# Kernel tuning notes

Measured on AMD Instinct MI355X. Metric: run time of the kernel, lower is better.

## Reference

```python
import jax, jax.numpy as jnp
import numpy as np

LEAKY_SLOPE = 0.2
LN_EPS = 1e-5


def _leaky_relu(x):
    return jnp.where(x >= 0, x, LEAKY_SLOPE * x)


def _layer_norm(x, gamma, beta):
    mean = jnp.mean(x, axis=-1, keepdims=True)
    var = jnp.var(x, axis=-1, keepdims=True)
    return (x - mean) * jax.lax.rsqrt(var + LN_EPS) * gamma + beta


def setup_inputs() -> dict:
    key = jax.random.key(0)
    ks = jax.random.split(key, 8)
    n_nodes, n_edges = 50000, 640000
    cin, cout = 128, 128
    x = jax.random.normal(ks[0], (n_nodes, cin), dtype=jnp.float32)
    edge_index = jax.random.randint(ks[1], (2, n_edges), 0, n_nodes, dtype=jnp.int64)
    # Linear weights stored torch-style [out, in]; init ~ U(-1/sqrt(fan_in), 1/sqrt(fan_in))
    def lin(k, fan_out, fan_in):
        b = 1.0 / np.sqrt(fan_in)
        return jax.random.uniform(k, (fan_out, fan_in), jnp.float32, -b, b)
    W1 = lin(ks[2], cout, 2 * cin)
    b1 = jax.random.uniform(ks[3], (cout,), jnp.float32, -1/np.sqrt(2*cin), 1/np.sqrt(2*cin))
    W2 = lin(ks[4], cout, cout)
    b2 = jax.random.uniform(ks[5], (cout,), jnp.float32, -1/np.sqrt(cout), 1/np.sqrt(cout))
    W3 = lin(ks[6], cout, cout)  # bias=False
    gamma = jnp.ones((cout,), jnp.float32)
    beta = jnp.zeros((cout,), jnp.float32)
    return {"x": x, "edge_index": edge_index, "W1": W1, "b1": b1,
            "W2": W2, "b2": b2, "W3": W3, "gamma": gamma, "beta": beta}


def reference(x, edge_index, W1, b1, W2, b2, W3, gamma, beta):
    src, dest = edge_index[0], edge_index[1]
    message = jnp.concatenate((x[dest], x[src]), axis=-1)  # [E, 2*cin]
    h = _leaky_relu(message @ W1.T + b1)
    h = _leaky_relu(h @ W2.T + b2)
    h = h @ W3.T
    return _layer_norm(h, gamma, beta)
```

## Files before the change

kernel.cpp:

```cpp
#include <hip/hip_runtime.h>

typedef unsigned short u16;
typedef unsigned int u32;
typedef __attribute__((ext_vector_type(8))) short bf16x8;
typedef __attribute__((ext_vector_type(4))) float f32x4;
typedef __attribute__((ext_vector_type(4))) u32 u32x4;

union U8 { u32 w[4]; u32x4 u4; bf16x8 v; };

#define LEAKY 0.2f
#define LN_EPS 1e-5f

__device__ __forceinline__ u16 f2bf(float f) {
  union { float f; u32 u; } a; a.f = f;
  return (u16)((a.u + 0x7fffu + ((a.u >> 16) & 1u)) >> 16);
}
__device__ __forceinline__ u32 pk2(float lo, float hi) {
  return (u32)f2bf(lo) | ((u32)f2bf(hi) << 16);
}
__device__ __forceinline__ u32x4 pack8(const f32x4& a, const f32x4& b) {
  u32x4 r;
  r[0] = pk2(a[0], a[1]); r[1] = pk2(a[2], a[3]);
  r[2] = pk2(b[0], b[1]); r[3] = pk2(b[2], b[3]);
  return r;
}

__global__ void build_wfrag(const float* __restrict__ W1,
                            const float* __restrict__ W2,
                            const float* __restrict__ W3,
                            u16* __restrict__ wout) {
  int id = blockIdx.x * 256 + threadIdx.x;
  int f = id >> 9, l = (id >> 3) & 63, i = id & 7;
  int p = l & 15, q = l >> 4, j = i & 3, h = i >> 2;
  const float* W; int c, K;
  if (f < 64)      { W = W1; c = f >> 3;        K = 256; }
  else if (f < 96) { W = W2; c = (f - 64) >> 3; K = 128; }
  else             { W = W3; c = (f - 96) >> 3; K = 128; }
  int n = f & 7;
  wout[id] = f2bf(W[(16 * n + p) * K + 32 * c + 4 * q + j + 16 * h]);
}

template <int FBASE>
__device__ __forceinline__ void gemm16(const u16* __restrict__ wlds, int lane,
                                       const U8* mf, f32x4* acc) {
  #pragma unroll
  for (int c = 0; c < 4; ++c) {
    #pragma unroll
    for (int n = 0; n < 8; ++n) {
      U8 wf;
      wf.v = *(const bf16x8*)(wlds + ((FBASE + c * 8 + n) << 9) + (lane << 3));
      acc[n] = __builtin_amdgcn_mfma_f32_16x16x32_bf16(wf.v, mf[c].v, acc[n], 0, 0, 0);
    }
  }
}

__device__ __forceinline__ void leaky_pack(f32x4* acc, U8* hf) {
  #pragma unroll
  for (int n = 0; n < 8; ++n) {
    #pragma unroll
    for (int j = 0; j < 4; ++j) {
      float v = acc[n][j];
      acc[n][j] = fmaxf(v, LEAKY * v);
    }
  }
  #pragma unroll
  for (int c = 0; c < 4; ++c) hf[c].u4 = pack8(acc[2 * c], acc[2 * c + 1]);
}

__device__ __forceinline__ u32 addleaky(u32 ua, u32 ub) {
  float alo = __uint_as_float(ua << 16);
  float ahi = __uint_as_float(ua & 0xFFFF0000u);
  float blo = __uint_as_float(ub << 16);
  float bhi = __uint_as_float(ub & 0xFFFF0000u);
  float lo = alo + blo, hi = ahi + bhi;
  lo = fmaxf(lo, LEAKY * lo);
  hi = fmaxf(hi, LEAKY * hi);
  return pk2(lo, hi);
}

__device__ __forceinline__ void ln_store(const f32x4* acc, const f32x4* gmf,
                                         const f32x4* btf, int q,
                                         float* __restrict__ orow) {
  float s = 0.f, ss = 0.f;
  #pragma unroll
  for (int n = 0; n < 8; ++n) {
    #pragma unroll
    for (int j = 0; j < 4; ++j) { float v = acc[n][j]; s += v; ss += v * v; }
  }
  s += __shfl_xor(s, 16, 64);  ss += __shfl_xor(ss, 16, 64);
  s += __shfl_xor(s, 32, 64);  ss += __shfl_xor(ss, 32, 64);
  float mean = s * (1.f / 128.f);
  float var  = fmaxf(ss * (1.f / 128.f) - mean * mean, 0.f);
  float inv  = rsqrtf(var + LN_EPS);
  #pragma unroll
  for (int n = 0; n < 8; ++n) {
    f32x4 gm = gmf[4 * n + q], bt = btf[4 * n + q];
    #pragma unroll
    for (int j = 0; j < 4; ++j)
      orow[16 * n + j] = (acc[n][j] - mean) * inv * gm[j] + bt[j];
  }
}

__global__ __launch_bounds__(512, 2) void node_pre(
    const float* __restrict__ x, const float* __restrict__ b1,
    const u16* __restrict__ wbf, u16* __restrict__ y, int NN) {
  __shared__ __align__(16) u16 wlds[32768];
  __shared__ __align__(16) float b1l[128];
  const int tid = threadIdx.x;
  {
    const uint4* s = (const uint4*)wbf;
    uint4* d = (uint4*)wlds;
    #pragma unroll
    for (int i = 0; i < 8; ++i) d[tid + i * 512] = s[tid + i * 512];
  }
  if (tid < 128) b1l[tid] = b1[tid];
  __syncthreads();

  const int lane = tid & 63, p = lane & 15, q = lane >> 4;
  const int wid = (blockIdx.x << 3) | (tid >> 6);
  const f32x4* b1f = (const f32x4*)b1l;
  const int NT = (NN + 15) >> 4;

  for (int t = wid; t < NT; t += 2048) {
    const int r = t * 16 + p;
    const int cr = r < NN ? r : NN - 1;
    U8 mf[4];
    #pragma unroll
    for (int c = 0; c < 4; ++c) {
      float4 a0 = *(const float4*)(x + (long)cr * 128 + 32 * c + 4 * q);
      float4 a1 = *(const float4*)(x + (long)cr * 128 + 32 * c + 4 * q + 16);
      mf[c].w[0] = pk2(a0.x, a0.y); mf[c].w[1] = pk2(a0.z, a0.w);
      mf[c].w[2] = pk2(a1.x, a1.y); mf[c].w[3] = pk2(a1.z, a1.w);
    }
    f32x4 ya[8], yb[8];
    #pragma unroll
    for (int n = 0; n < 8; ++n) {
      ya[n] = (f32x4)(0.f);
      yb[n] = b1f[4 * n + q];
    }
    gemm16<0>(wlds, lane, mf, ya);
    gemm16<32>(wlds, lane, mf, yb);
    #pragma unroll
    for (int c = 0; c < 4; ++c) {
      *(u32x4*)(y + (long)r * 256 + c * 32 + q * 8)       = pack8(ya[2*c], ya[2*c+1]);
      *(u32x4*)(y + (long)r * 256 + 128 + c * 32 + q * 8) = pack8(yb[2*c], yb[2*c+1]);
    }
  }
}

__global__ __launch_bounds__(512, 2) void edge_mlp_fac(
    const int* __restrict__ ei, const float* __restrict__ b2,
    const float* __restrict__ gamma, const float* __restrict__ beta,
    const u16* __restrict__ wbf, const u16* __restrict__ y,
    float* __restrict__ out, int E) {
  __shared__ __align__(16) u16 wlds[32768];
  __shared__ __align__(16) float parl[384];
  const int tid = threadIdx.x;
  {
    const uint4* s = (const uint4*)wbf;
    uint4* d = (uint4*)wlds;
    #pragma unroll
    for (int i = 0; i < 8; ++i) d[tid + i * 512] = s[tid + i * 512];
  }
  if (tid < 384) {
    int prm = tid >> 7, idx = tid & 127;
    const float* src = (prm == 0) ? b2 : (prm == 1) ? gamma : beta;
    parl[tid] = src[idx];
  }
  __syncthreads();

  const int lane = tid & 63, p = lane & 15, q = lane >> 4;
  const f32x4* pf = (const f32x4*)parl;
  const long ebase = (long)blockIdx.x * 512 + (tid >> 6) * 64;

  int nd[4], ns[4];
  #pragma unroll
  for (int i = 0; i < 4; ++i) {
    nd[i] = ei[E + ebase + i * 16 + p];
    ns[i] = ei[ebase + i * 16 + p];
  }

#define LOADY(A, B, node_d, node_s)                                   \
  { const u16* yd_ = y + (long)(node_d) * 256;                        \
    const u16* ys_ = y + (long)(node_s) * 256 + 128;                  \
    _Pragma("unroll")                                                 \
    for (int c = 0; c < 4; ++c) {                                     \
      A[c] = *(const u32x4*)(yd_ + c * 32 + q * 8);                   \
      B[c] = *(const u32x4*)(ys_ + c * 32 + q * 8);                   \
    } }

  auto compute_store = [&](const u32x4* ya, const u32x4* yb, int i) {
    U8 hf[4];
    #pragma unroll
    for (int c = 0; c < 4; ++c) {
      #pragma unroll
      for (int w2 = 0; w2 < 4; ++w2) hf[c].w[w2] = addleaky(ya[c][w2], yb[c][w2]);
    }
    f32x4 acc[8];
    #pragma unroll
    for (int n = 0; n < 8; ++n) acc[n] = pf[4 * n + q];
    gemm16<0>(wlds, lane, hf, acc);
    leaky_pack(acc, hf);
    #pragma unroll
    for (int n = 0; n < 8; ++n) acc[n] = (f32x4)(0.f);
    gemm16<32>(wlds, lane, hf, acc);
    ln_store(acc, pf + 32, pf + 64, q,
             out + (ebase + i * 16 + p) * 128 + 4 * q);
  };

  u32x4 a0[4], b0[4], a1[4], b1[4];
  LOADY(a0, b0, nd[0], ns[0]);
  LOADY(a1, b1, nd[1], ns[1]);
  compute_store(a0, b0, 0);
  LOADY(a0, b0, nd[2], ns[2]);
  compute_store(a1, b1, 1);
  LOADY(a1, b1, nd[3], ns[3]);
  compute_store(a0, b0, 2);
  compute_store(a1, b1, 3);
#undef LOADY
}

__global__ __launch_bounds__(512, 2) void edge_mlp_mono(
    const float* __restrict__ x, const int* __restrict__ ei,
    const float* __restrict__ b1, const float* __restrict__ b2,
    const float* __restrict__ gamma, const float* __restrict__ beta,
    const u16* __restrict__ wbf, float* __restrict__ out, int E) {
  __shared__ __align__(16) u16 wlds[65536];
  __shared__ __align__(16) float parl[512];
  const int tid = threadIdx.x;
  {
    const uint4* s = (const uint4*)wbf;
    uint4* d = (uint4*)wlds;
    #pragma unroll
    for (int i = 0; i < 16; ++i) d[tid + i * 512] = s[tid + i * 512];
  }
  if (tid < 512) {
    int prm = tid >> 7, idx = tid & 127;
    const float* src = (prm == 0) ? b1 : (prm == 1) ? b2 : (prm == 2) ? gamma : beta;
    parl[tid] = src[idx];
  }
  __syncthreads();

  const int lane = tid & 63, p = lane & 15, q = lane >> 4;
  const int wid = (blockIdx.x << 3) | (tid >> 6);
  const f32x4* pf = (const f32x4*)parl;
  const int NT = (E + 15) >> 4;

  for (int t = wid; t < NT; t += 2048) {
    const int e0 = t * 16;
    const int e = (e0 + p < E) ? e0 + p : E - 1;
    const int nd = ei[E + e], ns = ei[e];
    U8 mf[4];
    f32x4 acc[8];
    #pragma unroll
    for (int n = 0; n < 8; ++n) acc[n] = pf[4 * n + q];
    #pragma unroll
    for (int c = 0; c < 4; ++c) {
      float4 a0 = *(const float4*)(x + (long)nd * 128 + 32 * c + 4 * q);
      float4 a1 = *(const float4*)(x + (long)nd * 128 + 32 * c + 4 * q + 16);
      mf[c].w[0] = pk2(a0.x, a0.y); mf[c].w[1] = pk2(a0.z, a0.w);
      mf[c].w[2] = pk2(a1.x, a1.y); mf[c].w[3] = pk2(a1.z, a1.w);
    }
    gemm16<0>(wlds, lane, mf, acc);
    #pragma unroll
    for (int c = 0; c < 4; ++c) {
      float4 a0 = *(const float4*)(x + (long)ns * 128 + 32 * c + 4 * q);
      float4 a1 = *(const float4*)(x + (long)ns * 128 + 32 * c + 4 * q + 16);
      mf[c].w[0] = pk2(a0.x, a0.y); mf[c].w[1] = pk2(a0.z, a0.w);
      mf[c].w[2] = pk2(a1.x, a1.y); mf[c].w[3] = pk2(a1.z, a1.w);
    }
    gemm16<32>(wlds, lane, mf, acc);
    U8 hf[4];
    leaky_pack(acc, hf);
    #pragma unroll
    for (int n = 0; n < 8; ++n) acc[n] = pf[32 + 4 * n + q];
    gemm16<64>(wlds, lane, hf, acc);
    leaky_pack(acc, hf);
    #pragma unroll
    for (int n = 0; n < 8; ++n) acc[n] = (f32x4)(0.f);
    gemm16<96>(wlds, lane, hf, acc);
    if (e0 + p < E)
      ln_store(acc, pf + 64, pf + 96, q, out + (long)(e0 + p) * 128 + 4 * q);
  }
}

extern "C" void kernel_launch(void* const* d_in, const int* in_sizes, int n_in,
                              void* d_out, int out_size, void* d_ws, size_t ws_size,
                              hipStream_t stream) {
  const float* x     = (const float*)d_in[0];
  const int*   ei    = (const int*)d_in[1];
  const float* W1    = (const float*)d_in[2];
  const float* b1    = (const float*)d_in[3];
  const float* W2    = (const float*)d_in[4];
  const float* b2    = (const float*)d_in[5];
  const float* W3    = (const float*)d_in[6];
  const float* gamma = (const float*)d_in[7];
  const float* beta  = (const float*)d_in[8];
  const int E  = in_sizes[1] / 2;
  const int NN = in_sizes[0] / 128;

  const size_t npad    = ((size_t)(NN + 31) / 32) * 32;
  const size_t Y_BYTES = npad * 512;
  const size_t NEED    = Y_BYTES + 131072;

  if (ws_size >= NEED && (E % 512) == 0) {
    u16* y   = (u16*)d_ws;
    u16* wbf = (u16*)((char*)d_ws + Y_BYTES);
    build_wfrag<<<256, 256, 0, stream>>>(W1, W2, W3, wbf);
    node_pre<<<256, 512, 0, stream>>>(x, b1, wbf, y, NN);
    edge_mlp_fac<<<E / 512, 512, 0, stream>>>(ei, b2, gamma, beta, wbf + 32768,
                                              y, (float*)d_out, E);
  } else {
    u16* wbf = (u16*)d_ws;
    build_wfrag<<<256, 256, 0, stream>>>(W1, W2, W3, wbf);
    edge_mlp_mono<<<256, 512, 0, stream>>>(x, ei, b1, b2, gamma, beta, wbf,
                                           (float*)d_out, E);
  }
}
```

Measured before the change: 188.1 us.

## Process 1024 edges per block and issue first gathers before weight LDS load

Each block of edge_mlp_fac now handles 1024 edges instead of 512, with each wave processing eight 16-edge tiles in a double-buffered pipeline. Edge index loads are streamed just ahead of use rather than all preloaded. The first two gathers of node features are issued before the weight and parameter copy into LDS and the barrier, so gather latency overlaps the prologue. This halves the number of blocks and so the per-block cost of loading 64KB of weights into LDS. It also means fewer blocks for load balancing and requires E divisible by 1024; otherwise the slower fallback runs.

```diff
diff --git a/kernel.cpp b/kernel.cpp
--- a/kernel.cpp
+++ b/kernel.cpp
@@ -156,29 +156,9 @@
   __shared__ __align__(16) u16 wlds[32768];
   __shared__ __align__(16) float parl[384];
   const int tid = threadIdx.x;
-  {
-    const uint4* s = (const uint4*)wbf;
-    uint4* d = (uint4*)wlds;
-    #pragma unroll
-    for (int i = 0; i < 8; ++i) d[tid + i * 512] = s[tid + i * 512];
-  }
-  if (tid < 384) {
-    int prm = tid >> 7, idx = tid & 127;
-    const float* src = (prm == 0) ? b2 : (prm == 1) ? gamma : beta;
-    parl[tid] = src[idx];
-  }
-  __syncthreads();
-
   const int lane = tid & 63, p = lane & 15, q = lane >> 4;
   const f32x4* pf = (const f32x4*)parl;
-  const long ebase = (long)blockIdx.x * 512 + (tid >> 6) * 64;
-
-  int nd[4], ns[4];
-  #pragma unroll
-  for (int i = 0; i < 4; ++i) {
-    nd[i] = ei[E + ebase + i * 16 + p];
-    ns[i] = ei[ebase + i * 16 + p];
-  }
+  const long ebase = (long)blockIdx.x * 1024 + (tid >> 6) * 128;
 
 #define LOADY(A, B, node_d, node_s)                                   \
   { const u16* yd_ = y + (long)(node_d) * 256;                        \
@@ -189,6 +169,27 @@
       B[c] = *(const u32x4*)(ys_ + c * 32 + q * 8);                   \
     } }
 
+  int ndA = ei[E + ebase + p],      nsA = ei[ebase + p];
+  int ndB = ei[E + ebase + 16 + p], nsB = ei[ebase + 16 + p];
+  u32x4 a0[4], b0[4], a1[4], b1[4];
+  LOADY(a0, b0, ndA, nsA);
+  LOADY(a1, b1, ndB, nsB);
+  ndA = ei[E + ebase + 32 + p]; nsA = ei[ebase + 32 + p];
+  ndB = ei[E + ebase + 48 + p]; nsB = ei[ebase + 48 + p];
+
+  {
+    const uint4* s = (const uint4*)wbf;
+    uint4* d = (uint4*)wlds;
+    #pragma unroll
+    for (int i = 0; i < 8; ++i) d[tid + i * 512] = s[tid + i * 512];
+  }
+  if (tid < 384) {
+    int prm = tid >> 7, idx = tid & 127;
+    const float* src = (prm == 0) ? b2 : (prm == 1) ? gamma : beta;
+    parl[tid] = src[idx];
+  }
+  __syncthreads();
+
   auto compute_store = [&](const u32x4* ya, const u32x4* yb, int i) {
     U8 hf[4];
     #pragma unroll
@@ -208,15 +209,24 @@
              out + (ebase + i * 16 + p) * 128 + 4 * q);
   };
 
-  u32x4 a0[4], b0[4], a1[4], b1[4];
-  LOADY(a0, b0, nd[0], ns[0]);
-  LOADY(a1, b1, nd[1], ns[1]);
   compute_store(a0, b0, 0);
-  LOADY(a0, b0, nd[2], ns[2]);
+  LOADY(a0, b0, ndA, nsA);
+  ndA = ei[E + ebase + 64 + p]; nsA = ei[ebase + 64 + p];
   compute_store(a1, b1, 1);
-  LOADY(a1, b1, nd[3], ns[3]);
+  LOADY(a1, b1, ndB, nsB);
+  ndB = ei[E + ebase + 80 + p]; nsB = ei[ebase + 80 + p];
   compute_store(a0, b0, 2);
+  LOADY(a0, b0, ndA, nsA);
+  ndA = ei[E + ebase + 96 + p]; nsA = ei[ebase + 96 + p];
   compute_store(a1, b1, 3);
+  LOADY(a1, b1, ndB, nsB);
+  ndB = ei[E + ebase + 112 + p]; nsB = ei[ebase + 112 + p];
+  compute_store(a0, b0, 4);
+  LOADY(a0, b0, ndA, nsA);
+  compute_store(a1, b1, 5);
+  LOADY(a1, b1, ndB, nsB);
+  compute_store(a0, b0, 6);
+  compute_store(a1, b1, 7);
 #undef LOADY
 }
 
@@ -303,13 +313,13 @@
   const size_t Y_BYTES = npad * 512;
   const size_t NEED    = Y_BYTES + 131072;
 
-  if (ws_size >= NEED && (E % 512) == 0) {
+  if (ws_size >= NEED && (E % 1024) == 0) {
     u16* y   = (u16*)d_ws;
     u16* wbf = (u16*)((char*)d_ws + Y_BYTES);
     build_wfrag<<<256, 256, 0, stream>>>(W1, W2, W3, wbf);
     node_pre<<<256, 512, 0, stream>>>(x, b1, wbf, y, NN);
-    edge_mlp_fac<<<E / 512, 512, 0, stream>>>(ei, b2, gamma, beta, wbf + 32768,
-                                              y, (float*)d_out, E);
+    edge_mlp_fac<<<E / 1024, 512, 0, stream>>>(ei, b2, gamma, beta,
+                                               wbf + 32768, y, (float*)d_out, E);
   } else {
     u16* wbf = (u16*)d_ws;
     build_wfrag<<<256, 256, 0, stream>>>(W1, W2, W3, wbf);
```

After: 206.4 us. 9.7% more time.
